# Optimization experiments

Measured on AMD Instinct MI355X. Metric: run time of the kernel, lower is better.

The kernel has to match this reference:

```python
import jax, jax.numpy as jnp
import numpy as np

K = 512
DIM = 64


def setup_inputs() -> dict:
    key = jax.random.key(0)
    kx, ke = jax.random.split(key)
    x = jax.random.normal(kx, (64, 64, 32, 32), dtype=jnp.float32)  # (b, d, h, w)
    codebook = jax.random.normal(ke, (K, DIM), dtype=jnp.float32)  # nn.Embedding weight
    return {"x": x, "codebook": codebook}


def reference(x, codebook):
    b, d, h, w = x.shape
    # (b, d, h*w) -> (b, h*w, d)
    flat = jnp.transpose(x.reshape(b, d, h * w), (0, 2, 1))  # (b, n, d)
    x2 = jnp.sum(flat * flat, axis=-1, keepdims=True)              # (b, n, 1)
    e2 = jnp.sum(codebook * codebook, axis=-1)                     # (k,)
    xe = jnp.einsum('bnd,kd->bnk', flat, codebook)                 # (b, n, k)
    dist = x2 - 2.0 * xe + e2                                      # (b, n, k)
    idx = jnp.argmin(dist, axis=-1)                                # (b, n)
    quant = codebook[idx]                                          # (b, n, d) gather
    # straight-through estimator
    quant_st = flat + jax.lax.stop_gradient(quant - flat)
    out = jnp.transpose(quant_st, (0, 2, 1)).reshape(b, d, h, w)
    return out
```

## Files before the change

kernel.cpp:

```cpp
#include <hip/hip_runtime.h>

#define KCODES 512
#define DIM    64
#define NVEC   65536
#define TAU    0.05f

typedef __attribute__((ext_vector_type(8))) short   short8;
typedef __attribute__((ext_vector_type(4))) float   f32x4;

static __device__ __forceinline__ unsigned f2bfu(float f) {
    unsigned u = __builtin_bit_cast(unsigned, f);
    u += 0x7fffu + ((u >> 16) & 1u);
    return u >> 16;
}

__global__ void prep_kernel(const float* __restrict__ cb,
                            unsigned short* __restrict__ cbt,
                            float* __restrict__ e2q) {
    if (blockIdx.x < 128) {
        const int g   = blockIdx.x * 64 + threadIdx.x;
        const int s   = g >> 10;
        const int rem = g & 1023;
        const int h   = rem >> 9;
        const int qd  = (rem >> 6) & 7;
        const int cl  = rem & 63;
        const float* src = cb + (size_t)(s * 64 + cl) * DIM + qd * 8;
        short8 v;
#pragma unroll
        for (int j = 0; j < 8; ++j) {
            float f = src[j];
            unsigned u = __builtin_bit_cast(unsigned, f);
            if (h == 0) {
                v[j] = (short)(u >> 16);
            } else {
                float hi = __builtin_bit_cast(float, u & 0xFFFF0000u);
                v[j] = (short)f2bfu(f - hi);
            }
        }
        *(short8*)(cbt + (size_t)g * 8) = v;
    } else {
        const int k = blockIdx.x - 128;
        float v = cb[k * DIM + threadIdx.x];
        double p = (double)v * (double)v;
#pragma unroll
        for (int off = 32; off > 0; off >>= 1) p += __shfl_down(p, off, 64);
        if (threadIdx.x == 0) e2q[k] = (float)(0.5 * p + 256.0);
    }
}

__launch_bounds__(256, 3)
__global__ void vq_main(const float* __restrict__ x,
                        const float* __restrict__ cb,
                        const unsigned short* __restrict__ cbt,
                        const float* __restrict__ e2q,
                        float* __restrict__ out) {
    __shared__ __align__(16) unsigned short sA[2][8192];
    __shared__ __align__(16) unsigned char  sMix[16384];
    __shared__ float sE2[KCODES];

    unsigned short* sB = (unsigned short*)sMix;
    float* s_pf1 = (float*)sMix;
    float* s_pf2 = (float*)(sMix + 1024);
    int*   s_pi1 = (int*)(sMix + 2048);
    int*   s_pi2 = (int*)(sMix + 3072);
    int*   s_i1  = (int*)(sMix + 4096);
    int*   s_i2  = (int*)(sMix + 4352);
    int*   s_flag= (int*)(sMix + 4608);
    int*   s_win = (int*)(sMix + 4864);

    const int tid  = threadIdx.x;
    const int wave = tid >> 6;
    const int lane = tid & 63;
    const int quad = lane >> 4;
    const int l16  = lane & 15;

    const int v0    = blockIdx.x * 64;
    const int b     = v0 >> 10;
    const int nbase = v0 & 1023;
    const float* xb = x + (size_t)b * 65536;

    short8 stg[4];
#pragma unroll
    for (int r = 0; r < 4; ++r)
        stg[r] = *(const short8*)(cbt + (size_t)(tid + r * 256) * 8);

    {
        const int n_g = nbase + wave * 16 + l16;
#pragma unroll
        for (int ko = 0; ko < 2; ++ko) {
            short8 bh, bl;
#pragma unroll
            for (int j = 0; j < 8; ++j) {
                const int d = quad * 8 + j + ko * 32;
                float f = -xb[(size_t)d * 1024 + n_g];
                unsigned u = __builtin_bit_cast(unsigned, f);
                float hi = __builtin_bit_cast(float, u & 0xFFFF0000u);
                bh[j] = (short)(u >> 16);
                bl[j] = (short)f2bfu(f - hi);
            }
            *(short8*)(sB + (size_t)(wave * 256 +       ko * 64 + lane) * 8) = bh;
            *(short8*)(sB + (size_t)(wave * 256 + 128 + ko * 64 + lane) * 8) = bl;
        }
    }

    if (tid < 128) *(f32x4*)(sE2 + tid * 4) = *(const f32x4*)(e2q + tid * 4);
#pragma unroll
    for (int r = 0; r < 4; ++r)
        *(short8*)(sA[0] + (size_t)(tid + r * 256) * 8) = stg[r];
    __syncthreads();

    short8 Bh[4][2], Bl[4][2];
#pragma unroll
    for (int nt = 0; nt < 4; ++nt) {
#pragma unroll
        for (int ko = 0; ko < 2; ++ko) {
            Bh[nt][ko] = *(const short8*)(sB + (size_t)(nt * 256 +       ko * 64 + lane) * 8);
            Bl[nt][ko] = *(const short8*)(sB + (size_t)(nt * 256 + 128 + ko * 64 + lane) * 8);
        }
    }

    float f1[4], f2_[4];
    int   i1[4], i2_[4];
#pragma unroll
    for (int nt = 0; nt < 4; ++nt) {
        f1[nt] = 1e30f; f2_[nt] = 1e30f; i1[nt] = 0; i2_[nt] = 0;
    }

    const int roff = quad * 64 + wave * 16 + l16;

#pragma unroll 1
    for (int s = 0; s < 8; ++s) {
        if (s < 7) {
#pragma unroll
            for (int r = 0; r < 4; ++r)
                stg[r] = *(const short8*)(cbt +
                          (size_t)((s + 1) * 1024 + tid + r * 256) * 8);
        }

        const unsigned short* buf = sA[s & 1];
        short8 A00 = *(const short8*)(buf + (size_t)(      roff) * 8);
        short8 A01 = *(const short8*)(buf + (size_t)(256 + roff) * 8);
        short8 A10 = *(const short8*)(buf + (size_t)(512 + roff) * 8);
        short8 A11 = *(const short8*)(buf + (size_t)(768 + roff) * 8);
        const int cbase = s * 64 + wave * 16;
        const int idb   = cbase + quad * 4;
        f32x4 e2v = *(const f32x4*)(sE2 + cbase + quad * 4);

#pragma unroll
        for (int nt = 0; nt < 4; ++nt) {
            f32x4 acc = e2v;
            acc = __builtin_amdgcn_mfma_f32_16x16x32_bf16(A00, Bh[nt][0], acc, 0, 0, 0);
            acc = __builtin_amdgcn_mfma_f32_16x16x32_bf16(A01, Bh[nt][1], acc, 0, 0, 0);
            acc = __builtin_amdgcn_mfma_f32_16x16x32_bf16(A00, Bl[nt][0], acc, 0, 0, 0);
            acc = __builtin_amdgcn_mfma_f32_16x16x32_bf16(A01, Bl[nt][1], acc, 0, 0, 0);
            acc = __builtin_amdgcn_mfma_f32_16x16x32_bf16(A10, Bh[nt][0], acc, 0, 0, 0);
            acc = __builtin_amdgcn_mfma_f32_16x16x32_bf16(A11, Bh[nt][1], acc, 0, 0, 0);

#pragma unroll
            for (int r = 0; r < 4; ++r) {
                float dd = acc[r];
                int   id = idb + r;
                bool  c1 = dd < f1[nt];
                bool  c2 = dd < f2_[nt];
                i2_[nt] = c1 ? i1[nt] : (c2 ? id : i2_[nt]);
                f2_[nt] = fminf(fmaxf(f1[nt], dd), f2_[nt]);
                i1[nt]  = c1 ? id : i1[nt];
                f1[nt]  = fminf(f1[nt], dd);
            }
        }

        if (s < 7) {
#pragma unroll
            for (int r = 0; r < 4; ++r)
                *(short8*)(sA[(s + 1) & 1] + (size_t)(tid + r * 256) * 8) = stg[r];
        }
        __syncthreads();
    }

#pragma unroll
    for (int nt = 0; nt < 4; ++nt) {
        float F1 = f1[nt], F2 = f2_[nt];
        int   I1 = i1[nt], I2 = i2_[nt];
#pragma unroll
        for (int delta = 16; delta <= 32; delta <<= 1) {
            float of1 = __shfl_xor(F1, delta, 64);
            int   oi1 = __shfl_xor(I1, delta, 64);
            float of2 = __shfl_xor(F2, delta, 64);
            int   oi2 = __shfl_xor(I2, delta, 64);
            bool o1_first = (of1 < F1) || (of1 == F1 && oi1 < I1);
            if (o1_first) {
                bool keep = (F1 < of2) || (F1 == of2 && I1 < oi2);
                F2 = keep ? F1 : of2;
                I2 = keep ? I1 : oi2;
                F1 = of1; I1 = oi1;
            } else {
                bool o1_second = (of1 < F2) || (of1 == F2 && oi1 < I2);
                if (o1_second) { F2 = of1; I2 = oi1; }
            }
        }
        if (quad == 0) {
            const int v = nt * 16 + l16;
            s_pf1[v * 4 + wave] = F1;
            s_pf2[v * 4 + wave] = F2;
            s_pi1[v * 4 + wave] = I1;
            s_pi2[v * 4 + wave] = I2;
        }
    }
    __syncthreads();

    if (tid < 64) {
        const int v = tid;
        float F1 = s_pf1[v * 4 + 0], F2 = s_pf2[v * 4 + 0];
        int   I1 = s_pi1[v * 4 + 0], I2 = s_pi2[v * 4 + 0];
#pragma unroll
        for (int w = 1; w < 4; ++w) {
            float of1 = s_pf1[v * 4 + w], of2 = s_pf2[v * 4 + w];
            int   oi1 = s_pi1[v * 4 + w], oi2 = s_pi2[v * 4 + w];
            bool o1_first = (of1 < F1) || (of1 == F1 && oi1 < I1);
            if (o1_first) {
                bool keep = (F1 < of2) || (F1 == of2 && I1 < oi2);
                F2 = keep ? F1 : of2;
                I2 = keep ? I1 : oi2;
                F1 = of1; I1 = oi1;
            } else {
                bool o1_second = (of1 < F2) || (of1 == F2 && oi1 < I2);
                if (o1_second) { F2 = of1; I2 = oi1; }
            }
        }
        s_win[v]  = I1;
        s_i1[v]   = I1;
        s_i2[v]   = I2;
        s_flag[v] = (F2 - F1) < TAU;
    }
    __syncthreads();

    {
        const int vec = tid >> 2, sub = tid & 3;
        if (s_flag[vec]) {
            const int i1c = s_i1[vec], i2c = s_i2[vec];
            const float* xr = xb + nbase + vec;
            const float* r1 = cb + (size_t)i1c * DIM;
            const float* r2 = cb + (size_t)i2c * DIM;
            double D1 = 0.0, D2 = 0.0;
#pragma unroll 4
            for (int i = 0; i < 16; ++i) {
                const int d = sub + 4 * i;
                double xd = (double)xr[(size_t)d * 1024];
                double t1 = xd - (double)r1[d]; D1 += t1 * t1;
                double t2 = xd - (double)r2[d]; D2 += t2 * t2;
            }
            D1 += __shfl_down(D1, 2, 64); D1 += __shfl_down(D1, 1, 64);
            D2 += __shfl_down(D2, 2, 64); D2 += __shfl_down(D2, 1, 64);
            if (sub == 0) {
                if (D2 < D1 || (D2 == D1 && i2c < i1c)) s_win[vec] = i2c;
            }
        }
    }
    __syncthreads();

    {
        const int n    = tid & 63;
        const int dgrp = tid >> 6;
        const float4* crow = (const float4*)(cb + (size_t)s_win[n] * DIM);
        float* op = out + (size_t)b * 65536 + nbase + n;
#pragma unroll
        for (int i = 0; i < 4; ++i) {
            const int d0 = dgrp * 16 + i * 4;
            float4 val = crow[d0 >> 2];
            op[(size_t)(d0 + 0) * 1024] = val.x;
            op[(size_t)(d0 + 1) * 1024] = val.y;
            op[(size_t)(d0 + 2) * 1024] = val.z;
            op[(size_t)(d0 + 3) * 1024] = val.w;
        }
    }
}

extern "C" void kernel_launch(void* const* d_in, const int* in_sizes, int n_in,
                              void* d_out, int out_size, void* d_ws, size_t ws_size,
                              hipStream_t stream) {
    const float* x  = (const float*)d_in[0];
    const float* cb = (const float*)d_in[1];
    float* out = (float*)d_out;

    unsigned short* cbt = (unsigned short*)d_ws;
    float*          e2q = (float*)(cbt + 8192 * 8);

    prep_kernel<<<640, 64, 0, stream>>>(cb, cbt, e2q);
    vq_main<<<NVEC / 64, 256, 0, stream>>>(x, cb, cbt, e2q, out);
}
```

Measured before the change: 100.1 us.

## Stream codebook via direct global-to-LDS loads and retile waves 2x2

Codebook tile staging now goes straight from global memory into LDS through global_load_lds, so the register staging and the separate LDS store pass are gone. The 16KB mixed scratch buffer is removed and aliased onto the double-buffered codebook array, which cuts LDS use so the launch bound can rise to 4 blocks per CU. Waves are rearranged into a 2x2 grid (two vector tiles by two code subtiles), which halves the B fragments held in registers and halves the cross-wave merge. The costs are more A-fragment LDS reads per wave, an extra barrier, and reliance on correct aliasing between sB and the prefetch buffer.

```diff
diff --git a/kernel.cpp b/kernel.cpp
--- a/kernel.cpp
+++ b/kernel.cpp
@@ -12,6 +12,13 @@
     unsigned u = __builtin_bit_cast(unsigned, f);
     u += 0x7fffu + ((u >> 16) & 1u);
     return u >> 16;
+}
+
+static __device__ __forceinline__ void glds16(const unsigned short* g,
+                                              unsigned short* l) {
+    __builtin_amdgcn_global_load_lds(
+        (const __attribute__((address_space(1))) unsigned int*)g,
+        (__attribute__((address_space(3))) unsigned int*)l, 16, 0, 0);
 }
 
 __global__ void prep_kernel(const float* __restrict__ cb,
@@ -48,41 +55,43 @@
     }
 }
 
-__launch_bounds__(256, 3)
+__launch_bounds__(256, 4)
 __global__ void vq_main(const float* __restrict__ x,
                         const float* __restrict__ cb,
                         const unsigned short* __restrict__ cbt,
                         const float* __restrict__ e2q,
                         float* __restrict__ out) {
     __shared__ __align__(16) unsigned short sA[2][8192];
-    __shared__ __align__(16) unsigned char  sMix[16384];
     __shared__ float sE2[KCODES];
 
-    unsigned short* sB = (unsigned short*)sMix;
-    float* s_pf1 = (float*)sMix;
-    float* s_pf2 = (float*)(sMix + 1024);
-    int*   s_pi1 = (int*)(sMix + 2048);
-    int*   s_pi2 = (int*)(sMix + 3072);
-    int*   s_i1  = (int*)(sMix + 4096);
-    int*   s_i2  = (int*)(sMix + 4352);
-    int*   s_flag= (int*)(sMix + 4608);
-    int*   s_win = (int*)(sMix + 4864);
+    unsigned short* sB = sA[1];
+    unsigned char* scr = (unsigned char*)sA[0];
+    float* s_pf1 = (float*)(scr);
+    float* s_pf2 = (float*)(scr + 512);
+    int*   s_pi1 = (int*)(scr + 1024);
+    int*   s_pi2 = (int*)(scr + 1536);
+    int*   s_i1  = (int*)(scr + 2048);
+    int*   s_i2  = (int*)(scr + 2304);
+    int*   s_flag= (int*)(scr + 2560);
+    int*   s_win = (int*)(scr + 2816);
 
     const int tid  = threadIdx.x;
     const int wave = tid >> 6;
     const int lane = tid & 63;
     const int quad = lane >> 4;
     const int l16  = lane & 15;
+    const int wr   = wave >> 1;
+    const int wc   = wave & 1;
 
     const int v0    = blockIdx.x * 64;
     const int b     = v0 >> 10;
     const int nbase = v0 & 1023;
     const float* xb = x + (size_t)b * 65536;
 
-    short8 stg[4];
 #pragma unroll
     for (int r = 0; r < 4; ++r)
-        stg[r] = *(const short8*)(cbt + (size_t)(tid + r * 256) * 8);
+        glds16(cbt + (size_t)(r * 256 + wave * 64 + lane) * 8,
+               sA[0] + (size_t)(r * 256 + wave * 64) * 8);
 
     {
         const int n_g = nbase + wave * 16 + l16;
@@ -104,83 +113,78 @@
     }
 
     if (tid < 128) *(f32x4*)(sE2 + tid * 4) = *(const f32x4*)(e2q + tid * 4);
-#pragma unroll
-    for (int r = 0; r < 4; ++r)
-        *(short8*)(sA[0] + (size_t)(tid + r * 256) * 8) = stg[r];
-    __syncthreads();
-
-    short8 Bh[4][2], Bl[4][2];
-#pragma unroll
-    for (int nt = 0; nt < 4; ++nt) {
+    __syncthreads();
+
+    short8 Bh[2][2], Bl[2][2];
+#pragma unroll
+    for (int t = 0; t < 2; ++t) {
+        const int tile = 2 * wr + t;
 #pragma unroll
         for (int ko = 0; ko < 2; ++ko) {
-            Bh[nt][ko] = *(const short8*)(sB + (size_t)(nt * 256 +       ko * 64 + lane) * 8);
-            Bl[nt][ko] = *(const short8*)(sB + (size_t)(nt * 256 + 128 + ko * 64 + lane) * 8);
-        }
-    }
-
-    float f1[4], f2_[4];
-    int   i1[4], i2_[4];
-#pragma unroll
-    for (int nt = 0; nt < 4; ++nt) {
-        f1[nt] = 1e30f; f2_[nt] = 1e30f; i1[nt] = 0; i2_[nt] = 0;
-    }
-
-    const int roff = quad * 64 + wave * 16 + l16;
+            Bh[t][ko] = *(const short8*)(sB + (size_t)(tile * 256 +       ko * 64 + lane) * 8);
+            Bl[t][ko] = *(const short8*)(sB + (size_t)(tile * 256 + 128 + ko * 64 + lane) * 8);
+        }
+    }
+    __syncthreads();
+
+    float f1[2], f2_[2];
+    int   i1[2], i2_[2];
+#pragma unroll
+    for (int t = 0; t < 2; ++t) {
+        f1[t] = 1e30f; f2_[t] = 1e30f; i1[t] = 0; i2_[t] = 0;
+    }
 
 #pragma unroll 1
     for (int s = 0; s < 8; ++s) {
         if (s < 7) {
 #pragma unroll
             for (int r = 0; r < 4; ++r)
-                stg[r] = *(const short8*)(cbt +
-                          (size_t)((s + 1) * 1024 + tid + r * 256) * 8);
+                glds16(cbt + (size_t)((s + 1) * 1024 + r * 256 + wave * 64 + lane) * 8,
+                       sA[(s + 1) & 1] + (size_t)(r * 256 + wave * 64) * 8);
         }
 
         const unsigned short* buf = sA[s & 1];
-        short8 A00 = *(const short8*)(buf + (size_t)(      roff) * 8);
-        short8 A01 = *(const short8*)(buf + (size_t)(256 + roff) * 8);
-        short8 A10 = *(const short8*)(buf + (size_t)(512 + roff) * 8);
-        short8 A11 = *(const short8*)(buf + (size_t)(768 + roff) * 8);
-        const int cbase = s * 64 + wave * 16;
-        const int idb   = cbase + quad * 4;
-        f32x4 e2v = *(const f32x4*)(sE2 + cbase + quad * 4);
-
-#pragma unroll
-        for (int nt = 0; nt < 4; ++nt) {
-            f32x4 acc = e2v;
-            acc = __builtin_amdgcn_mfma_f32_16x16x32_bf16(A00, Bh[nt][0], acc, 0, 0, 0);
-            acc = __builtin_amdgcn_mfma_f32_16x16x32_bf16(A01, Bh[nt][1], acc, 0, 0, 0);
-            acc = __builtin_amdgcn_mfma_f32_16x16x32_bf16(A00, Bl[nt][0], acc, 0, 0, 0);
-            acc = __builtin_amdgcn_mfma_f32_16x16x32_bf16(A01, Bl[nt][1], acc, 0, 0, 0);
-            acc = __builtin_amdgcn_mfma_f32_16x16x32_bf16(A10, Bh[nt][0], acc, 0, 0, 0);
-            acc = __builtin_amdgcn_mfma_f32_16x16x32_bf16(A11, Bh[nt][1], acc, 0, 0, 0);
-
-#pragma unroll
-            for (int r = 0; r < 4; ++r) {
-                float dd = acc[r];
-                int   id = idb + r;
-                bool  c1 = dd < f1[nt];
-                bool  c2 = dd < f2_[nt];
-                i2_[nt] = c1 ? i1[nt] : (c2 ? id : i2_[nt]);
-                f2_[nt] = fminf(fmaxf(f1[nt], dd), f2_[nt]);
-                i1[nt]  = c1 ? id : i1[nt];
-                f1[nt]  = fminf(f1[nt], dd);
-            }
-        }
-
-        if (s < 7) {
-#pragma unroll
-            for (int r = 0; r < 4; ++r)
-                *(short8*)(sA[(s + 1) & 1] + (size_t)(tid + r * 256) * 8) = stg[r];
+#pragma unroll
+        for (int st = 0; st < 2; ++st) {
+            const int roff  = quad * 64 + wc * 32 + st * 16 + l16;
+            short8 A00 = *(const short8*)(buf + (size_t)(      roff) * 8);
+            short8 A01 = *(const short8*)(buf + (size_t)(256 + roff) * 8);
+            short8 A10 = *(const short8*)(buf + (size_t)(512 + roff) * 8);
+            short8 A11 = *(const short8*)(buf + (size_t)(768 + roff) * 8);
+            const int cbase = s * 64 + wc * 32 + st * 16;
+            const int idb   = cbase + quad * 4;
+            f32x4 e2v = *(const f32x4*)(sE2 + idb);
+
+#pragma unroll
+            for (int t = 0; t < 2; ++t) {
+                f32x4 acc = e2v;
+                acc = __builtin_amdgcn_mfma_f32_16x16x32_bf16(A00, Bh[t][0], acc, 0, 0, 0);
+                acc = __builtin_amdgcn_mfma_f32_16x16x32_bf16(A01, Bh[t][1], acc, 0, 0, 0);
+                acc = __builtin_amdgcn_mfma_f32_16x16x32_bf16(A00, Bl[t][0], acc, 0, 0, 0);
+                acc = __builtin_amdgcn_mfma_f32_16x16x32_bf16(A01, Bl[t][1], acc, 0, 0, 0);
+                acc = __builtin_amdgcn_mfma_f32_16x16x32_bf16(A10, Bh[t][0], acc, 0, 0, 0);
+                acc = __builtin_amdgcn_mfma_f32_16x16x32_bf16(A11, Bh[t][1], acc, 0, 0, 0);
+
+#pragma unroll
+                for (int r = 0; r < 4; ++r) {
+                    float dd = acc[r];
+                    int   id = idb + r;
+                    bool  c1 = dd < f1[t];
+                    bool  c2 = dd < f2_[t];
+                    i2_[t] = c1 ? i1[t] : (c2 ? id : i2_[t]);
+                    f2_[t] = fminf(fmaxf(f1[t], dd), f2_[t]);
+                    i1[t]  = c1 ? id : i1[t];
+                    f1[t]  = fminf(f1[t], dd);
+                }
+            }
         }
         __syncthreads();
     }
 
 #pragma unroll
-    for (int nt = 0; nt < 4; ++nt) {
-        float F1 = f1[nt], F2 = f2_[nt];
-        int   I1 = i1[nt], I2 = i2_[nt];
+    for (int t = 0; t < 2; ++t) {
+        float F1 = f1[t], F2 = f2_[t];
+        int   I1 = i1[t], I2 = i2_[t];
 #pragma unroll
         for (int delta = 16; delta <= 32; delta <<= 1) {
             float of1 = __shfl_xor(F1, delta, 64);
@@ -199,23 +203,22 @@
             }
         }
         if (quad == 0) {
-            const int v = nt * 16 + l16;
-            s_pf1[v * 4 + wave] = F1;
-            s_pf2[v * 4 + wave] = F2;
-            s_pi1[v * 4 + wave] = I1;
-            s_pi2[v * 4 + wave] = I2;
+            const int v = wr * 32 + t * 16 + l16;
+            s_pf1[v * 2 + wc] = F1;
+            s_pf2[v * 2 + wc] = F2;
+            s_pi1[v * 2 + wc] = I1;
+            s_pi2[v * 2 + wc] = I2;
         }
     }
     __syncthreads();
 
     if (tid < 64) {
         const int v = tid;
-        float F1 = s_pf1[v * 4 + 0], F2 = s_pf2[v * 4 + 0];
-        int   I1 = s_pi1[v * 4 + 0], I2 = s_pi2[v * 4 + 0];
-#pragma unroll
-        for (int w = 1; w < 4; ++w) {
-            float of1 = s_pf1[v * 4 + w], of2 = s_pf2[v * 4 + w];
-            int   oi1 = s_pi1[v * 4 + w], oi2 = s_pi2[v * 4 + w];
+        float F1 = s_pf1[v * 2 + 0], F2 = s_pf2[v * 2 + 0];
+        int   I1 = s_pi1[v * 2 + 0], I2 = s_pi2[v * 2 + 0];
+        {
+            float of1 = s_pf1[v * 2 + 1], of2 = s_pf2[v * 2 + 1];
+            int   oi1 = s_pi1[v * 2 + 1], oi2 = s_pi2[v * 2 + 1];
             bool o1_first = (of1 < F1) || (of1 == F1 && oi1 < I1);
             if (o1_first) {
                 bool keep = (F1 < of2) || (F1 == of2 && I1 < oi2);
```

New measurement: 94.59 us. 5.5% less time.
